# Optimization experiments

Measured on AMD Instinct MI355X. Metric: run time of the kernel, lower is better.

## Reference

```python
import jax, jax.numpy as jnp
import numpy as np

B, S, D, H = 2, 2048, 1024, 16
HD = D // H  # head_dim = 64
NEG = -1.0e9


def setup_inputs() -> dict:
    key = jax.random.key(0)
    ks = jax.random.split(key, 9)
    s = 1.0 / np.sqrt(D)
    return {
        "x": jax.random.normal(ks[0], (B, S, D), jnp.float32),
        "mask": jnp.ones((B, S), jnp.float32),
        "Wq": jax.random.normal(ks[1], (D, D), jnp.float32) * s,
        "bq": jnp.zeros((D,), jnp.float32),
        "Wk": jax.random.normal(ks[2], (D, D), jnp.float32) * s,
        "bk": jnp.zeros((D,), jnp.float32),
        "Wv": jax.random.normal(ks[3], (D, D), jnp.float32) * s,
        "bv": jnp.zeros((D,), jnp.float32),
        "Wo": jax.random.normal(ks[4], (D, D), jnp.float32) * s,
        "bo": jnp.zeros((D,), jnp.float32),
    }


def reference(x, mask, Wq, bq, Wk, bk, Wv, bv, Wo, bo):
    # QKV projections -> [B, H, S, HD]
    def proj(t, W, b):
        return (t @ W + b).reshape(B, S, H, HD).transpose(0, 2, 1, 3)

    q = proj(x, Wq, bq)
    k = proj(x, Wk, bk)
    v = proj(x, Wv, bv)

    scores = jnp.einsum("bhqd,bhkd->bhqk", q, k) / jnp.sqrt(jnp.asarray(HD, x.dtype))
    # causal mask: scores * m + (1-m) * -1e9 (matches original exactly)
    cm = jnp.tril(jnp.ones((S, S), x.dtype))[None, None]
    scores = scores * cm + (1.0 - cm) * NEG
    # 2D padding mask branch
    scores = scores + (1.0 - mask[:, None, None, :]) * NEG

    attn = jax.nn.softmax(scores, axis=-1)
    out = jnp.einsum("bhqk,bhkd->bqhd", attn, v).reshape(B, S, D)
    return out @ Wo + bo
```

## Files before the change

kernel.cpp:

```cpp
#include <hip/hip_runtime.h>
#include <hip/hip_bf16.h>
#include <cstdint>
#include <cstddef>

typedef __attribute__((ext_vector_type(8))) short short8;
typedef __attribute__((ext_vector_type(4))) float floatx4;
typedef __attribute__((ext_vector_type(2))) unsigned int uintx2;
typedef __attribute__((ext_vector_type(4))) unsigned int uintx4;

#define MFMA16(a, b, c) __builtin_amdgcn_mfma_f32_16x16x32_bf16((a), (b), (c), 0, 0, 0)
#define LOG2E 1.44269504088896340736f
#define EXP2(x) __builtin_amdgcn_exp2f(x)

__device__ __forceinline__ unsigned short f2bf(float f) {
  unsigned int u = __builtin_bit_cast(unsigned int, f);
  u += 0x7fffu + ((u >> 16) & 1u);
  return (unsigned short)(u >> 16);
}

__device__ __forceinline__ unsigned int pk2(float a, float b) {
  float2 f; f.x = a; f.y = b;
  __hip_bfloat162 h = __float22bfloat162_rn(f);
  unsigned int u;
  __builtin_memcpy(&u, &h, 4);
  return u;
}

typedef __attribute__((address_space(1))) void gvoid_t;
typedef __attribute__((address_space(3))) void svoid_t;
__device__ __forceinline__ void gload_lds16(const void* g, void* l) {
  __builtin_amdgcn_global_load_lds((gvoid_t*)(uintptr_t)g, (svoid_t*)(uintptr_t)l, 16, 0, 0);
}

__global__ void convert_x(const float* __restrict__ x, unsigned short* __restrict__ xb) {
  int i = (blockIdx.x * 256 + threadIdx.x) * 4;
  floatx4 v = *(const floatx4*)(x + i);
  uintx2 o;
  o[0] = pk2(v[0], v[1]);
  o[1] = pk2(v[2], v[3]);
  *(uintx2*)(xb + i) = o;
}

__global__ void transpose_w(const float* __restrict__ Wq, const float* __restrict__ Wk,
                            const float* __restrict__ Wv, const float* __restrict__ Wo,
                            unsigned short* __restrict__ Wqkvt, unsigned short* __restrict__ Wot) {
  __shared__ float tile[32][33];
  int z = blockIdx.z;
  const float* W = (z == 0) ? Wq : (z == 1) ? Wk : (z == 2) ? Wv : Wo;
  unsigned short* out = (z == 3) ? Wot : (Wqkvt + (size_t)z * 1024 * 1024);
  int n0 = blockIdx.x * 32, k0 = blockIdx.y * 32;
  int tx = threadIdx.x, ty = threadIdx.y;
#pragma unroll
  for (int j = 0; j < 4; ++j)
    tile[ty + j * 8][tx] = W[(size_t)(k0 + ty + j * 8) * 1024 + n0 + tx];
  __syncthreads();
#pragma unroll
  for (int j = 0; j < 4; ++j)
    out[(size_t)(n0 + ty + j * 8) * 1024 + k0 + tx] = f2bf(tile[tx][ty + j * 8]);
}

#define GEMM_PROLOGUE128()                                                     \
  __shared__ __align__(16) unsigned short Sh[2 * 128 * 64];                    \
  unsigned short* const As = Sh;                                               \
  unsigned short* const Bs = Sh + 128 * 64;                                    \
  const int tid = threadIdx.x;                                                 \
  const int lane = tid & 63;                                                   \
  const int wid = tid >> 6;                                                    \
  const int col = lane & 15;                                                   \
  const int quad = lane >> 4;                                                  \
  const int m0 = blockIdx.x * 128;                                             \
  const int n0 = blockIdx.y * 128;                                             \
  const int wm = wid >> 1;                                                     \
  const int wn = wid & 1;                                                      \
  floatx4 acc[4][4];                                                           \
  _Pragma("unroll") for (int i = 0; i < 4; ++i)                                \
      _Pragma("unroll") for (int j = 0; j < 4; ++j)                            \
          acc[i][j] = (floatx4)(0.f);                                          \
  _Pragma("unroll 1") for (int kt = 0; kt < 16; ++kt) {                        \
    __syncthreads();                                                           \
    _Pragma("unroll") for (int call = 0; call < 4; ++call) {                   \
      int c = call * 256 + tid;                                                \
      int r = c >> 3, ch = c & 7;                                              \
      gload_lds16(A + (size_t)(m0 + r) * 1024 + kt * 64 + ((ch ^ (r & 7)) * 8),\
                  As + (size_t)(call * 256 + wid * 64) * 8);                   \
      gload_lds16(Bt + (size_t)(n0 + r) * 1024 + kt * 64 + ((ch ^ (r & 7)) * 8),\
                  Bs + (size_t)(call * 256 + wid * 64) * 8);                   \
    }                                                                          \
    __syncthreads();                                                           \
    _Pragma("unroll") for (int ks = 0; ks < 2; ++ks) {                         \
      short8 af[4], bf[4];                                                     \
      _Pragma("unroll") for (int rt = 0; rt < 4; ++rt) {                       \
        int row = wm * 64 + rt * 16 + col;                                     \
        af[rt] = *(const short8*)&As[row * 64 + (((ks * 4 + quad) ^ (row & 7)) * 8)]; \
      }                                                                        \
      _Pragma("unroll") for (int ct = 0; ct < 4; ++ct) {                       \
        int row = wn * 64 + ct * 16 + col;                                     \
        bf[ct] = *(const short8*)&Bs[row * 64 + (((ks * 4 + quad) ^ (row & 7)) * 8)]; \
      }                                                                        \
      _Pragma("unroll") for (int rt = 0; rt < 4; ++rt)                         \
          _Pragma("unroll") for (int ct = 0; ct < 4; ++ct)                     \
              acc[rt][ct] = MFMA16(af[rt], bf[ct], acc[rt][ct]);               \
    }                                                                          \
  }

#define GEMM_PROLOGUE64()                                                      \
  __shared__ __align__(16) unsigned short As[64 * 64];                         \
  __shared__ __align__(16) unsigned short Bs[128 * 64];                        \
  const int tid = threadIdx.x;                                                 \
  const int lane = tid & 63;                                                   \
  const int wid = tid >> 6;                                                    \
  const int col = lane & 15;                                                   \
  const int quad = lane >> 4;                                                  \
  const int m0 = blockIdx.x * 64;                                              \
  const int n0 = blockIdx.y * 128;                                             \
  const int wm = wid >> 1;                                                     \
  const int wn = wid & 1;                                                      \
  floatx4 acc[2][4];                                                           \
  _Pragma("unroll") for (int i = 0; i < 2; ++i)                                \
      _Pragma("unroll") for (int j = 0; j < 4; ++j)                            \
          acc[i][j] = (floatx4)(0.f);                                          \
  _Pragma("unroll 1") for (int kt = 0; kt < 16; ++kt) {                        \
    __syncthreads();                                                           \
    _Pragma("unroll") for (int call = 0; call < 2; ++call) {                   \
      int c = call * 256 + tid;                                                \
      int r = c >> 3, ch = c & 7;                                              \
      gload_lds16(A + (size_t)(m0 + r) * 1024 + kt * 64 + ((ch ^ (r & 7)) * 8),\
                  As + (size_t)(call * 256 + wid * 64) * 8);                   \
    }                                                                          \
    _Pragma("unroll") for (int call = 0; call < 4; ++call) {                   \
      int c = call * 256 + tid;                                                \
      int r = c >> 3, ch = c & 7;                                              \
      gload_lds16(Bt + (size_t)(n0 + r) * 1024 + kt * 64 + ((ch ^ (r & 7)) * 8),\
                  Bs + (size_t)(call * 256 + wid * 64) * 8);                   \
    }                                                                          \
    __syncthreads();                                                           \
    _Pragma("unroll") for (int ks = 0; ks < 2; ++ks) {                         \
      short8 af[2], bf[4];                                                     \
      _Pragma("unroll") for (int rt = 0; rt < 2; ++rt) {                       \
        int row = wm * 32 + rt * 16 + col;                                     \
        af[rt] = *(const short8*)&As[row * 64 + (((ks * 4 + quad) ^ (row & 7)) * 8)]; \
      }                                                                        \
      _Pragma("unroll") for (int ct = 0; ct < 4; ++ct) {                       \
        int row = wn * 64 + ct * 16 + col;                                     \
        bf[ct] = *(const short8*)&Bs[row * 64 + (((ks * 4 + quad) ^ (row & 7)) * 8)]; \
      }                                                                        \
      _Pragma("unroll") for (int rt = 0; rt < 2; ++rt)                         \
          _Pragma("unroll") for (int ct = 0; ct < 4; ++ct)                     \
              acc[rt][ct] = MFMA16(af[rt], bf[ct], acc[rt][ct]);               \
    }                                                                          \
  }

__global__ __launch_bounds__(256, 3)
void gemm_qkv(const unsigned short* __restrict__ A, const unsigned short* __restrict__ Bt,
              const float* __restrict__ bq, const float* __restrict__ bk,
              const float* __restrict__ bv,
              unsigned short* __restrict__ Qo, unsigned short* __restrict__ Ko,
              unsigned short* __restrict__ Vo) {
  GEMM_PROLOGUE128()
  const int nseg = n0 >> 10;
  const float* bias = (nseg == 0) ? bq : ((nseg == 1) ? bk : bv);
  if (nseg == 2) {
    __syncthreads();
    const int cb = n0 & 1023;
#pragma unroll
    for (int rt = 0; rt < 4; ++rt) {
#pragma unroll
      for (int ct = 0; ct < 4; ++ct) {
        int cl = wn * 64 + ct * 16 + col;
        int mb = wm * 16 + rt * 4 + quad;
        float bb = bias[cb + cl];
        uintx2 w;
        w[0] = pk2(acc[rt][ct][0] + bb, acc[rt][ct][1] + bb);
        w[1] = pk2(acc[rt][ct][2] + bb, acc[rt][ct][3] + bb);
        *(uintx2*)&Sh[cl * 128 + ((mb ^ (cl & 31)) * 4)] = w;
      }
    }
    __syncthreads();
    {
      int cl = tid >> 1, half = tid & 1;
      int hh = (cb >> 6) + (cl >> 6);
      int hd = cl & 63;
      int b_ = m0 >> 11;
      int s0 = (m0 & 2047) + half * 64;
      unsigned short* dst = Vo + (size_t)(b_ * 16 + hh) * 131072 + (size_t)hd * 2048 + s0;
#pragma unroll
      for (int k = 0; k < 8; ++k) {
        int mb0 = half * 16 + k * 2;
        uintx2 lo = *(const uintx2*)&Sh[cl * 128 + ((mb0 ^ (cl & 31)) * 4)];
        uintx2 hi = *(const uintx2*)&Sh[cl * 128 + (((mb0 + 1) ^ (cl & 31)) * 4)];
        uintx4 v;
        v[0] = lo[0]; v[1] = lo[1]; v[2] = hi[0]; v[3] = hi[1];
        *(uintx4*)&dst[k * 8] = v;
      }
    }
  } else {
#pragma unroll
    for (int rt = 0; rt < 4; ++rt) {
#pragma unroll
      for (int ct = 0; ct < 4; ++ct) {
        int mg = m0 + wm * 64 + rt * 16 + quad * 4;
        int ng = n0 + wn * 64 + ct * 16 + col;
        int c = ng & 1023;
        int hh = c >> 6, hd = c & 63;
        int b_ = mg >> 11, s = mg & 2047;
        float bb = bias[c];
        unsigned short* dst =
            ((nseg == 0) ? Qo : Ko) + ((size_t)(b_ * 16 + hh) * 2048 + s) * 64 + hd;
        float scl = (nseg == 0) ? (0.125f * LOG2E) : 1.0f;
#pragma unroll
        for (int i = 0; i < 4; ++i) dst[(size_t)i * 64] = f2bf((acc[rt][ct][i] + bb) * scl);
      }
    }
  }
}

__global__ __launch_bounds__(256, 5)
void gemm_out(const unsigned short* __restrict__ A, const unsigned short* __restrict__ Bt,
              const float* __restrict__ bo, float* __restrict__ Out) {
  GEMM_PROLOGUE64()
#pragma unroll
  for (int rt = 0; rt < 2; ++rt) {
#pragma unroll
    for (int ct = 0; ct < 4; ++ct) {
      int mg = m0 + wm * 32 + rt * 16 + quad * 4;
      int ng = n0 + wn * 64 + ct * 16 + col;
      float bb = bo[ng];
#pragma unroll
      for (int i = 0; i < 4; ++i)
        Out[(size_t)(mg + i) * 1024 + ng] = acc[rt][ct][i] + bb;
    }
  }
}

__global__ __launch_bounds__(256, 4)
void flash_attn(const unsigned short* __restrict__ Q, const unsigned short* __restrict__ K,
                const unsigned short* __restrict__ Vt, const float* __restrict__ mask,
                unsigned short* __restrict__ O) {
  __shared__ __align__(16) unsigned short Ks[128 * 64];
  __shared__ __align__(16) unsigned short Vs[64 * 128];

  const int tid = threadIdx.x;
  const int lane = tid & 63;
  const int wid = tid >> 6;
  const int col = lane & 15;
  const int quad = lane >> 4;
  const int slot = (int)(blockIdx.x >> 8);
  const int g = (int)(blockIdx.x & 255);
  const int h8 = g >> 5;
  const int bh = g & 31;
  const int j = (slot == 0) ? (31 - h8) : (slot == 1) ? h8 : (slot == 2) ? (23 - h8) : (8 + h8);
  const int b = bh >> 4, h = bh & 15;
  const int q0 = j * 64;
  const int tdiag = j >> 1;

  const unsigned short* Qp = Q + (size_t)bh * 2048 * 64;
  const unsigned short* Kp = K + (size_t)bh * 2048 * 64;
  const unsigned short* Vp = Vt + (size_t)bh * 64 * 2048;
  const float* mp = mask + b * 2048;

  const int lr8 = lane >> 3, lc8 = lane & 7;
  const int lr16 = lane >> 4, lc16 = lane & 15;
  const floatx4 fzero = (floatx4)(0.f);
  const floatx4 fone = (floatx4)(1.f);
  const short8 ones8 = (short8)(short)0x3F80;

#pragma unroll
  for (int i = 0; i < 2; ++i) {
    int seg = wid * 2 + i;
    int r = seg * 8 + lr8;
    gload_lds16(Qp + (size_t)(q0 + r) * 64 + ((lc8 ^ (r & 7)) * 8), Ks + seg * 512);
  }
  __syncthreads();
  short8 qf[2];
  {
    int q = wid * 16 + col;
#pragma unroll
    for (int ks = 0; ks < 2; ++ks)
      qf[ks] = *(const short8*)&Ks[q * 64 + (((ks * 4 + quad) ^ (q & 7)) * 8)];
  }
  unsigned int mbits = 0;
  for (int t = 0; t <= tdiag; ++t) {
    float2 mv = *(const float2*)&mp[t * 128 + lane * 2];
    unsigned long long bb = __ballot(mv.x != 1.f || mv.y != 1.f);
    mbits |= (bb ? 1u : 0u) << t;
  }

  floatx4 o[4];
#pragma unroll
  for (int dt = 0; dt < 4; ++dt) o[dt] = fzero;
  float mrow = -1e30f;
  float lrow = 0.f;

#pragma unroll 1
  for (int t = 0; t <= tdiag; ++t) {
    __syncthreads();
#pragma unroll
    for (int i = 0; i < 4; ++i) {
      int seg = wid * 4 + i;
      int r = seg * 8 + lr8;
      gload_lds16(Kp + (size_t)(t * 128 + r) * 64 + ((lc8 ^ (r & 7)) * 8), Ks + seg * 512);
    }
#pragma unroll
    for (int i = 0; i < 4; ++i) {
      int seg = wid * 4 + i;
      int r = seg * 4 + lr16;
      gload_lds16(Vp + (size_t)r * 2048 + t * 128 + ((lc16 ^ (r & 15)) * 8), Vs + seg * 512);
    }
    __syncthreads();

    floatx4 sc[8];
    __builtin_amdgcn_s_setprio(1);
#pragma unroll
    for (int rt = 0; rt < 8; ++rt) {
      int kr = rt * 16 + col;
      short8 kf0 = *(const short8*)&Ks[kr * 64 + ((quad ^ (col & 7)) * 8)];
      short8 kf1 = *(const short8*)&Ks[kr * 64 + (((4 + quad) ^ (col & 7)) * 8)];
      floatx4 s0 = MFMA16(kf0, qf[0], fzero);
      sc[rt] = MFMA16(kf1, qf[1], s0);
    }
    __builtin_amdgcn_s_setprio(0);
    __syncthreads();

    if (__builtin_amdgcn_readfirstlane(mbits >> t) & 1) {
#pragma unroll
      for (int rt = 0; rt < 8; ++rt) {
        floatx4 mm = *(const floatx4*)&mp[t * 128 + rt * 16 + quad * 4];
        sc[rt] += (fone - mm) * (-1.0e9f * LOG2E);
      }
    }
    if (t == tdiag) {
      int qg = q0 + wid * 16 + col;
#pragma unroll
      for (int rt = 0; rt < 8; ++rt)
#pragma unroll
        for (int i = 0; i < 4; ++i)
          if (t * 128 + rt * 16 + quad * 4 + i > qg) sc[rt][i] = -1.0e9f * LOG2E;
    }

    float mt = -1e30f;
#pragma unroll
    for (int rt = 0; rt < 8; ++rt)
      mt = fmaxf(mt, fmaxf(fmaxf(sc[rt][0], sc[rt][1]), fmaxf(sc[rt][2], sc[rt][3])));
    mt = fmaxf(mt, __shfl_xor(mt, 16));
    mt = fmaxf(mt, __shfl_xor(mt, 32));

    const bool skip = (__all(mt - mrow <= 8.0f) != 0);
    float mn = mrow;
    if (!skip) {
      mn = fmaxf(mrow, mt);
      float alpha = EXP2(mrow - mn);
      mrow = mn;
      lrow *= alpha;
#pragma unroll
      for (int dt = 0; dt < 4; ++dt) o[dt] *= alpha;
    }
#pragma unroll
    for (int rt = 0; rt < 8; ++rt)
#pragma unroll
      for (int i = 0; i < 4; ++i) sc[rt][i] = EXP2(sc[rt][i] - mn);

    {
      int qloc = wid * 16 + col;
#pragma unroll
      for (int rt = 0; rt < 8; ++rt) {
        uintx2 w;
        w[0] = pk2(sc[rt][0], sc[rt][1]);
        w[1] = pk2(sc[rt][2], sc[rt][3]);
        int chunk = (rt * 2 + (quad >> 1)) ^ col;
        *(uintx2*)&Ks[qloc * 128 + chunk * 8 + (quad & 1) * 4] = w;
      }
    }
    floatx4 ssum = fzero;
    __builtin_amdgcn_s_setprio(1);
#pragma unroll
    for (int ks = 0; ks < 4; ++ks) {
      int ch = ks * 4 + quad;
      short8 pf = *(const short8*)&Ks[(wid * 16 + col) * 128 + ((ch ^ col) * 8)];
      ssum = MFMA16(ones8, pf, ssum);
#pragma unroll
      for (int dt = 0; dt < 4; ++dt) {
        short8 vf = *(const short8*)&Vs[(dt * 16 + col) * 128 + ((ch ^ col) * 8)];
        o[dt] = MFMA16(vf, pf, o[dt]);
      }
    }
    __builtin_amdgcn_s_setprio(0);
    lrow += ssum[0];
  }

  {
    float inv = 1.0f / lrow;
    int qg = q0 + wid * 16 + col;
    unsigned short* dst = O + ((size_t)(b * 2048 + qg)) * 1024 + h * 64;
#pragma unroll
    for (int dt = 0; dt < 4; ++dt) {
      uintx2 pk;
      pk[0] = pk2(o[dt][0] * inv, o[dt][1] * inv);
      pk[1] = pk2(o[dt][2] * inv, o[dt][3] * inv);
      *(uintx2*)&dst[dt * 16 + quad * 4] = pk;
    }
  }
}

extern "C" void kernel_launch(void* const* d_in, const int* in_sizes, int n_in,
                              void* d_out, int out_size, void* d_ws, size_t ws_size,
                              hipStream_t stream) {
  (void)in_sizes; (void)n_in; (void)out_size; (void)ws_size;
  const float* x  = (const float*)d_in[0];
  const float* mask = (const float*)d_in[1];
  const float* Wq = (const float*)d_in[2];
  const float* bq = (const float*)d_in[3];
  const float* Wk = (const float*)d_in[4];
  const float* bk = (const float*)d_in[5];
  const float* Wv = (const float*)d_in[6];
  const float* bv = (const float*)d_in[7];
  const float* Wo = (const float*)d_in[8];
  const float* bo = (const float*)d_in[9];
  float* out = (float*)d_out;

  char* ws = (char*)d_ws;
  unsigned short* xb    = (unsigned short*)(ws);
  unsigned short* Wqkvt = (unsigned short*)(ws + (8u << 20));
  unsigned short* Wot   = (unsigned short*)(ws + (14u << 20));
  unsigned short* Qb    = (unsigned short*)(ws + (16u << 20));
  unsigned short* Kb    = (unsigned short*)(ws + (24u << 20));
  unsigned short* Vtb   = (unsigned short*)(ws + (32u << 20));
  unsigned short* Ao    = (unsigned short*)(ws + (40u << 20));

  convert_x<<<4096, 256, 0, stream>>>(x, xb);
  transpose_w<<<dim3(32, 32, 4), dim3(32, 8), 0, stream>>>(Wq, Wk, Wv, Wo, Wqkvt, Wot);
  gemm_qkv<<<dim3(32, 24), 256, 0, stream>>>(xb, Wqkvt, bq, bk, bv, Qb, Kb, Vtb);
  flash_attn<<<dim3(1024), 256, 0, stream>>>(Qb, Kb, Vtb, mask, Ao);
  gemm_out<<<dim3(64, 8), 256, 0, stream>>>(Ao, Wot, bo, out);
}
```

Baseline: 182.8 us.

## Process 128 query rows per attention block to reuse K/V tiles

The flash attention kernel now handles 128 queries per block, 32 per wave in two 16-row chunks, instead of 64. The grid shrinks from 1024 to 512 blocks, and each loaded 128-key K/V tile is reused across twice as many queries, which halves K/V global-to-LDS traffic and the barriers per query. V fragments are hoisted into registers and reused for both chunks, and each wave writes P into its own LDS slab. The cost is much higher register pressure, with launch bounds relaxed to 2 blocks per CU, and fewer blocks to balance the causal workload.

```diff
diff --git a/kernel.cpp b/kernel.cpp
--- a/kernel.cpp
+++ b/kernel.cpp
@@ -232,7 +232,7 @@
   }
 }
 
-__global__ __launch_bounds__(256, 4)
+__global__ __launch_bounds__(256, 2)
 void flash_attn(const unsigned short* __restrict__ Q, const unsigned short* __restrict__ K,
                 const unsigned short* __restrict__ Vt, const float* __restrict__ mask,
                 unsigned short* __restrict__ O) {
@@ -244,14 +244,15 @@
   const int wid = tid >> 6;
   const int col = lane & 15;
   const int quad = lane >> 4;
-  const int slot = (int)(blockIdx.x >> 8);
-  const int g = (int)(blockIdx.x & 255);
-  const int h8 = g >> 5;
-  const int bh = g & 31;
-  const int j = (slot == 0) ? (31 - h8) : (slot == 1) ? h8 : (slot == 2) ? (23 - h8) : (8 + h8);
+
+  const int u = (int)blockIdx.x & 255;
+  const int half = (int)blockIdx.x >> 8;
+  const int jj = u >> 5;
+  const int j = half ? jj : (15 - jj);
+  const int bh = u & 31;
   const int b = bh >> 4, h = bh & 15;
-  const int q0 = j * 64;
-  const int tdiag = j >> 1;
+  const int q0 = j * 128;
+  const int nt = j + 1;
 
   const unsigned short* Qp = Q + (size_t)bh * 2048 * 64;
   const unsigned short* Kp = K + (size_t)bh * 2048 * 64;
@@ -265,34 +266,40 @@
   const short8 ones8 = (short8)(short)0x3F80;
 
 #pragma unroll
-  for (int i = 0; i < 2; ++i) {
-    int seg = wid * 2 + i;
-    int r = seg * 8 + lr8;
-    gload_lds16(Qp + (size_t)(q0 + r) * 64 + ((lc8 ^ (r & 7)) * 8), Ks + seg * 512);
+  for (int i = 0; i < 4; ++i) {
+    int c = i * 256 + tid;
+    int r = c >> 3, ch = c & 7;
+    gload_lds16(Qp + (size_t)(q0 + r) * 64 + ((ch ^ (r & 7)) * 8),
+                Ks + (size_t)(i * 256 + wid * 64) * 8);
   }
   __syncthreads();
-  short8 qf[2];
-  {
-    int q = wid * 16 + col;
+  short8 qf[2][2];
+#pragma unroll
+  for (int qc = 0; qc < 2; ++qc) {
+    int q = wid * 32 + qc * 16 + col;
 #pragma unroll
     for (int ks = 0; ks < 2; ++ks)
-      qf[ks] = *(const short8*)&Ks[q * 64 + (((ks * 4 + quad) ^ (q & 7)) * 8)];
+      qf[ks][qc] = *(const short8*)&Ks[q * 64 + (((ks * 4 + quad) ^ (q & 7)) * 8)];
   }
   unsigned int mbits = 0;
-  for (int t = 0; t <= tdiag; ++t) {
+  for (int t = 0; t < nt; ++t) {
     float2 mv = *(const float2*)&mp[t * 128 + lane * 2];
     unsigned long long bb = __ballot(mv.x != 1.f || mv.y != 1.f);
     mbits |= (bb ? 1u : 0u) << t;
   }
 
-  floatx4 o[4];
-#pragma unroll
-  for (int dt = 0; dt < 4; ++dt) o[dt] = fzero;
-  float mrow = -1e30f;
-  float lrow = 0.f;
+  floatx4 o[4][2];
+#pragma unroll
+  for (int dt = 0; dt < 4; ++dt) {
+    o[dt][0] = fzero;
+    o[dt][1] = fzero;
+  }
+  float mrow[2] = {-1e30f, -1e30f};
+  float lrow[2] = {0.f, 0.f};
+  unsigned short* slab = Ks + wid * 2048;
 
 #pragma unroll 1
-  for (int t = 0; t <= tdiag; ++t) {
+  for (int t = 0; t < nt; ++t) {
     __syncthreads();
 #pragma unroll
     for (int i = 0; i < 4; ++i) {
@@ -308,15 +315,18 @@
     }
     __syncthreads();
 
-    floatx4 sc[8];
+    floatx4 sc[8][2];
     __builtin_amdgcn_s_setprio(1);
 #pragma unroll
     for (int rt = 0; rt < 8; ++rt) {
       int kr = rt * 16 + col;
       short8 kf0 = *(const short8*)&Ks[kr * 64 + ((quad ^ (col & 7)) * 8)];
       short8 kf1 = *(const short8*)&Ks[kr * 64 + (((4 + quad) ^ (col & 7)) * 8)];
-      floatx4 s0 = MFMA16(kf0, qf[0], fzero);
-      sc[rt] = MFMA16(kf1, qf[1], s0);
+#pragma unroll
+      for (int qc = 0; qc < 2; ++qc) {
+        floatx4 s0 = MFMA16(kf0, qf[0][qc], fzero);
+        sc[rt][qc] = MFMA16(kf1, qf[1][qc], s0);
+      }
     }
     __builtin_amdgcn_s_setprio(0);
     __syncthreads();
@@ -325,77 +335,97 @@
 #pragma unroll
       for (int rt = 0; rt < 8; ++rt) {
         floatx4 mm = *(const floatx4*)&mp[t * 128 + rt * 16 + quad * 4];
-        sc[rt] += (fone - mm) * (-1.0e9f * LOG2E);
-      }
-    }
-    if (t == tdiag) {
-      int qg = q0 + wid * 16 + col;
+        floatx4 bias = (fone - mm) * (-1.0e9f * LOG2E);
+        sc[rt][0] += bias;
+        sc[rt][1] += bias;
+      }
+    }
+    if (t == j) {
+#pragma unroll
+      for (int qc = 0; qc < 2; ++qc) {
+        int qg = q0 + wid * 32 + qc * 16 + col;
+#pragma unroll
+        for (int rt = 0; rt < 8; ++rt)
+#pragma unroll
+          for (int i = 0; i < 4; ++i)
+            if (t * 128 + rt * 16 + quad * 4 + i > qg) sc[rt][qc][i] = -1.0e9f * LOG2E;
+      }
+    }
+
+    unsigned int pw[8][2][2];
+#pragma unroll
+    for (int qc = 0; qc < 2; ++qc) {
+      float mt = -1e30f;
 #pragma unroll
       for (int rt = 0; rt < 8; ++rt)
-#pragma unroll
-        for (int i = 0; i < 4; ++i)
-          if (t * 128 + rt * 16 + quad * 4 + i > qg) sc[rt][i] = -1.0e9f * LOG2E;
-    }
-
-    float mt = -1e30f;
-#pragma unroll
-    for (int rt = 0; rt < 8; ++rt)
-      mt = fmaxf(mt, fmaxf(fmaxf(sc[rt][0], sc[rt][1]), fmaxf(sc[rt][2], sc[rt][3])));
-    mt = fmaxf(mt, __shfl_xor(mt, 16));
-    mt = fmaxf(mt, __shfl_xor(mt, 32));
-
-    const bool skip = (__all(mt - mrow <= 8.0f) != 0);
-    float mn = mrow;
-    if (!skip) {
-      mn = fmaxf(mrow, mt);
-      float alpha = EXP2(mrow - mn);
-      mrow = mn;
-      lrow *= alpha;
-#pragma unroll
-      for (int dt = 0; dt < 4; ++dt) o[dt] *= alpha;
-    }
-#pragma unroll
-    for (int rt = 0; rt < 8; ++rt)
-#pragma unroll
-      for (int i = 0; i < 4; ++i) sc[rt][i] = EXP2(sc[rt][i] - mn);
-
-    {
-      int qloc = wid * 16 + col;
+        mt = fmaxf(mt, fmaxf(fmaxf(sc[rt][qc][0], sc[rt][qc][1]),
+                             fmaxf(sc[rt][qc][2], sc[rt][qc][3])));
+      mt = fmaxf(mt, __shfl_xor(mt, 16));
+      mt = fmaxf(mt, __shfl_xor(mt, 32));
+      const bool skip = (__all(mt - mrow[qc] <= 8.0f) != 0);
+      float mn = mrow[qc];
+      if (!skip) {
+        mn = fmaxf(mrow[qc], mt);
+        float alpha = EXP2(mrow[qc] - mn);
+        mrow[qc] = mn;
+        lrow[qc] *= alpha;
+#pragma unroll
+        for (int dt = 0; dt < 4; ++dt) o[dt][qc] *= alpha;
+      }
+#pragma unroll
+      for (int rt = 0; rt < 8; ++rt)
+#pragma unroll
+        for (int i = 0; i < 4; ++i) sc[rt][qc][i] = EXP2(sc[rt][qc][i] - mn);
+#pragma unroll
+      for (int rt = 0; rt < 8; ++rt) {
+        pw[rt][qc][0] = pk2(sc[rt][qc][0], sc[rt][qc][1]);
+        pw[rt][qc][1] = pk2(sc[rt][qc][2], sc[rt][qc][3]);
+      }
+    }
+
+    short8 vf[4][4];
+#pragma unroll
+    for (int ks = 0; ks < 4; ++ks)
+#pragma unroll
+      for (int dt = 0; dt < 4; ++dt)
+        vf[ks][dt] = *(const short8*)&Vs[(dt * 16 + col) * 128 + ((((ks * 4 + quad)) ^ col) * 8)];
+
+    __builtin_amdgcn_s_setprio(1);
+#pragma unroll
+    for (int qc = 0; qc < 2; ++qc) {
 #pragma unroll
       for (int rt = 0; rt < 8; ++rt) {
         uintx2 w;
-        w[0] = pk2(sc[rt][0], sc[rt][1]);
-        w[1] = pk2(sc[rt][2], sc[rt][3]);
+        w[0] = pw[rt][qc][0];
+        w[1] = pw[rt][qc][1];
         int chunk = (rt * 2 + (quad >> 1)) ^ col;
-        *(uintx2*)&Ks[qloc * 128 + chunk * 8 + (quad & 1) * 4] = w;
-      }
-    }
-    floatx4 ssum = fzero;
-    __builtin_amdgcn_s_setprio(1);
-#pragma unroll
-    for (int ks = 0; ks < 4; ++ks) {
-      int ch = ks * 4 + quad;
-      short8 pf = *(const short8*)&Ks[(wid * 16 + col) * 128 + ((ch ^ col) * 8)];
-      ssum = MFMA16(ones8, pf, ssum);
-#pragma unroll
-      for (int dt = 0; dt < 4; ++dt) {
-        short8 vf = *(const short8*)&Vs[(dt * 16 + col) * 128 + ((ch ^ col) * 8)];
-        o[dt] = MFMA16(vf, pf, o[dt]);
-      }
+        *(uintx2*)&slab[col * 128 + chunk * 8 + (quad & 1) * 4] = w;
+      }
+      floatx4 ssum = fzero;
+#pragma unroll
+      for (int ks = 0; ks < 4; ++ks) {
+        int ch = ks * 4 + quad;
+        short8 pf = *(const short8*)&slab[col * 128 + ((ch ^ col) * 8)];
+        ssum = MFMA16(ones8, pf, ssum);
+#pragma unroll
+        for (int dt = 0; dt < 4; ++dt)
+          o[dt][qc] = MFMA16(vf[ks][dt], pf, o[dt][qc]);
+      }
+      lrow[qc] += ssum[0];
     }
     __builtin_amdgcn_s_setprio(0);
-    lrow += ssum[0];
-  }
-
-  {
-    float inv = 1.0f / lrow;
-    int qg = q0 + wid * 16 + col;
+  }
+
+#pragma unroll
+  for (int qc = 0; qc < 2; ++qc) {
+    float inv = 1.0f / lrow[qc];
+    int qg = q0 + wid * 32 + qc * 16 + col;
     unsigned short* dst = O + ((size_t)(b * 2048 + qg)) * 1024 + h * 64;
 #pragma unroll
     for (int dt = 0; dt < 4; ++dt) {
       uintx2 pk;
-      pk[0] = pk2(o[dt][0] * inv, o[dt][1] * inv);
-      pk[1] = pk2(o[dt][2] * inv, o[dt][3] * inv);
+      pk[0] = pk2(o[dt][qc][0] * inv, o[dt][qc][1] * inv);
+      pk[1] = pk2(o[dt][qc][2] * inv, o[dt][qc][3] * inv);
       *(uintx2*)&dst[dt * 16 + quad * 4] = pk;
     }
   }
@@ -429,6 +459,6 @@
   convert_x<<<4096, 256, 0, stream>>>(x, xb);
   transpose_w<<<dim3(32, 32, 4), dim3(32, 8), 0, stream>>>(Wq, Wk, Wv, Wo, Wqkvt, Wot);
   gemm_qkv<<<dim3(32, 24), 256, 0, stream>>>(xb, Wqkvt, bq, bk, bv, Qb, Kb, Vtb);
-  flash_attn<<<dim3(1024), 256, 0, stream>>>(Qb, Kb, Vtb, mask, Ao);
+  flash_attn<<<dim3(512), 256, 0, stream>>>(Qb, Kb, Vtb, mask, Ao);
   gemm_out<<<dim3(64, 8), 256, 0, stream>>>(Ao, Wot, bo, out);
 }
```

Result: slower. 187.8 us (+2.7%).
